# Optimization experiments

Hardware: AMD Instinct MI355X
Metric: run time of the kernel (lower is better)

## Reference

```python
import jax, jax.numpy as jnp
import numpy as np

LAMBDA_GEO = 0.5


def setup_inputs() -> dict:
    key = jax.random.key(0)
    embeddings = jax.random.normal(key, (4, 2048, 512), dtype=jnp.float32)
    return {"embeddings": embeddings}


def _geometric_loss(embeddings):
    b, s, d = embeddings.shape
    x = embeddings.reshape(b * s, d)  # [N, d]
    sq_norm = jnp.sum(x * x, axis=-1)  # [N]
    sq = sq_norm[:, None] + sq_norm[None, :] - 2.0 * (x @ x.T)  # [N, N]
    sq = jnp.maximum(sq, 0.0)
    dist = jnp.sqrt(sq)  # torch.cdist(p=2)
    return jnp.mean(jnp.exp(-dist * 0.1)) * 0.1


def reference(embeddings):
    geometric_loss = _geometric_loss(embeddings)
    total_geometric = LAMBDA_GEO * geometric_loss
    return geometric_loss, total_geometric
```

## Files before the change

kernel.cpp:

```cpp
#include <hip/hip_runtime.h>

#define NROWS 8192
#define DIM   512
#define NT    64
#define NTRI  (NT * (NT + 1) / 2)
#define NACC  64

using f32x4 = __attribute__((ext_vector_type(4))) float;

__device__ __forceinline__ unsigned char f2e4m3(float x) {
    unsigned ux = __float_as_uint(x);
    unsigned s  = (ux >> 24) & 0x80u;
    float a = __uint_as_float(ux & 0x7FFFFFFFu);
    a = fminf(a, 448.0f);
    unsigned ua = __float_as_uint(a);
    int eb = (int)(ua >> 23);
    if (eb < 121) eb = 121;
    float step  = __uint_as_float((unsigned)(eb - 3) << 23);
    float istep = __uint_as_float((unsigned)(257 - eb) << 23);
    float q = rintf(a * istep) * step;
    q = fminf(q, 448.0f);
    if (q < 0.001953125f)
        return (unsigned char)s;
    unsigned uq = __float_as_uint(q);
    int eq = (int)(uq >> 23) - 127;
    unsigned byte;
    if (eq < -6) byte = (unsigned)(q * 512.0f);
    else         byte = (unsigned)((eq + 7) << 3) | ((uq >> 20) & 7u);
    return (unsigned char)(s | byte);
}

__global__ __launch_bounds__(256) void norm_convert_kernel(
    const float* __restrict__ X, unsigned char* __restrict__ Xq,
    float* __restrict__ norms, float* __restrict__ acc)
{
    const int tid  = threadIdx.x;
    const int lane = tid & 63;
    const int w    = tid >> 6;
    const int row  = blockIdx.x * 4 + w;

    if (blockIdx.x == 0 && tid < NACC) acc[tid] = 0.0f;

    const float* xr = X + (size_t)row * DIM + lane * 8;
    float4 v0 = *(const float4*)xr;
    float4 v1 = *(const float4*)(xr + 4);

    float s = 0.0f;
    s = fmaf(v0.x, v0.x, s); s = fmaf(v0.y, v0.y, s);
    s = fmaf(v0.z, v0.z, s); s = fmaf(v0.w, v0.w, s);
    s = fmaf(v1.x, v1.x, s); s = fmaf(v1.y, v1.y, s);
    s = fmaf(v1.z, v1.z, s); s = fmaf(v1.w, v1.w, s);

    union { unsigned char b[8]; uint2 v; } pk;
    pk.b[0] = f2e4m3(v0.x); pk.b[1] = f2e4m3(v0.y);
    pk.b[2] = f2e4m3(v0.z); pk.b[3] = f2e4m3(v0.w);
    pk.b[4] = f2e4m3(v1.x); pk.b[5] = f2e4m3(v1.y);
    pk.b[6] = f2e4m3(v1.z); pk.b[7] = f2e4m3(v1.w);

    const int slab = lane >> 3;
    const int cpos = (lane & 7) ^ (row & 7);
    *(uint2*)(Xq + (size_t)row * DIM + slab * 64 + cpos * 8) = pk.v;

    #pragma unroll
    for (int off = 32; off > 0; off >>= 1) s += __shfl_down(s, off, 64);
    if (lane == 0) norms[row] = s;
}

__global__ __launch_bounds__(256, 4) void pair_loss_gemm_kernel(
    const unsigned char* __restrict__ Xq, const float* __restrict__ norms,
    float* __restrict__ acc)
{
    __shared__ __align__(16) char As0[8192];
    __shared__ __align__(16) char As1[8192];
    __shared__ __align__(16) char Bs0[8192];
    __shared__ __align__(16) char Bs1[8192];
    __shared__ float wsum[4];

    int t = blockIdx.x, bi = 0;
    while (t >= (NT - bi)) { t -= (NT - bi); bi++; }
    const int bj = bi + t;

    const int tid  = threadIdx.x;
    const int lane = tid & 63;
    const int w    = tid >> 6;

    const int rowA = bi * 128;
    const int rowB = bj * 128;

    f32x4 accv[4][4];
    const f32x4 zero = {0.0f, 0.0f, 0.0f, 0.0f};
    #pragma unroll
    for (int a = 0; a < 4; a++)
        #pragma unroll
        for (int b = 0; b < 4; b++) accv[a][b] = zero;

    const int r0 = tid >> 1;
    const int h0 = tid & 1;
    const int wb = r0 * 64 + h0 * 32;
    const unsigned char* gA = Xq + (size_t)(rowA + r0) * DIM + h0 * 32;
    const unsigned char* gB = Xq + (size_t)(rowB + r0) * DIM + h0 * 32;

    const int fr  = lane & 15;
    const int q   = lane >> 4;
    const int fo0 = fr * 64 + ((q ^ (fr & 7)) * 8);
    const int wr  = (w & 1) * 64;
    const int wc  = (w >> 1) * 64;

    {
        uint4 pa0 = *(const uint4*)gA;
        uint4 pa1 = *(const uint4*)(gA + 16);
        uint4 pb0 = *(const uint4*)gB;
        uint4 pb1 = *(const uint4*)(gB + 16);
        *(uint4*)(As0 + wb)      = pa0;
        *(uint4*)(As0 + wb + 16) = pa1;
        *(uint4*)(Bs0 + wb)      = pb0;
        *(uint4*)(Bs0 + wb + 16) = pb1;
    }
    __syncthreads();

    char* curA = As0; char* nxtA = As1;
    char* curB = Bs0; char* nxtB = Bs1;

    #pragma unroll 1
    for (int k = 0; k < 8; k++) {
        uint4 pa0, pa1, pb0, pb1;
        const bool more = (k < 7);
        if (more) {
            const int k0 = (k + 1) * 64;
            pa0 = *(const uint4*)(gA + k0);
            pa1 = *(const uint4*)(gA + k0 + 16);
            pb0 = *(const uint4*)(gB + k0);
            pb1 = *(const uint4*)(gB + k0 + 16);
        }

        #pragma unroll
        for (int s = 0; s < 2; s++) {
            const int fo = fo0 ^ (s << 5);
            long af[4], bf[4];
            #pragma unroll
            for (int a = 0; a < 4; a++)
                af[a] = *(const long*)(curA + (wr + a * 16) * 64 + fo);
            #pragma unroll
            for (int b = 0; b < 4; b++)
                bf[b] = *(const long*)(curB + (wc + b * 16) * 64 + fo);
            #pragma unroll
            for (int a = 0; a < 4; a++)
                #pragma unroll
                for (int b = 0; b < 4; b++)
                    accv[a][b] = __builtin_amdgcn_mfma_f32_16x16x32_fp8_fp8(
                        af[a], bf[b], accv[a][b], 0, 0, 0);
        }

        if (more) {
            *(uint4*)(nxtA + wb)      = pa0;
            *(uint4*)(nxtA + wb + 16) = pa1;
            *(uint4*)(nxtB + wb)      = pb0;
            *(uint4*)(nxtB + wb + 16) = pb1;
            __syncthreads();
            char* tA = curA; curA = nxtA; nxtA = tA;
            char* tB = curB; curB = nxtB; nxtB = tB;
        }
    }

    const float wgt = (bi == bj) ? 1.0f : 2.0f;
    float lsum = 0.0f;
    #pragma unroll
    for (int a = 0; a < 4; a++) {
        const int gi0 = rowA + wr + a * 16 + (lane >> 4) * 4;
        #pragma unroll
        for (int b = 0; b < 4; b++) {
            const int gj = rowB + wc + b * 16 + (lane & 15);
            const float nj = norms[gj];
            #pragma unroll
            for (int r = 0; r < 4; r++) {
                const int gi = gi0 + r;
                float sq = fmaf(-2.0f, accv[a][b][r], norms[gi] + nj);
                sq = fmaxf(sq, 0.0f);
                float term = __expf(-0.1f * sqrtf(sq));
                if (gi == gj) term = 1.0f;
                lsum += term;
            }
        }
    }
    lsum *= wgt;
    #pragma unroll
    for (int off = 32; off > 0; off >>= 1) lsum += __shfl_down(lsum, off, 64);
    if (lane == 0) wsum[w] = lsum;
    __syncthreads();
    if (tid == 0)
        atomicAdd(&acc[blockIdx.x & (NACC - 1)],
                  wsum[0] + wsum[1] + wsum[2] + wsum[3]);
}

__global__ void finalize_kernel(const float* __restrict__ acc,
                                float* __restrict__ out)
{
    const int lane = threadIdx.x;
    float s = (lane < NACC) ? acc[lane] : 0.0f;
    #pragma unroll
    for (int off = 32; off > 0; off >>= 1) s += __shfl_down(s, off, 64);
    if (lane == 0) {
        const float inv = 1.0f / ((float)NROWS * (float)NROWS);
        float loss = s * inv * 0.1f;
        out[0] = loss;
        out[1] = 0.5f * loss;
    }
}

extern "C" void kernel_launch(void* const* d_in, const int* in_sizes, int n_in,
                              void* d_out, int out_size, void* d_ws, size_t ws_size,
                              hipStream_t stream)
{
    const float* X = (const float*)d_in[0];
    float* out = (float*)d_out;

    char* ws = (char*)d_ws;
    float*         acc   = (float*)ws;
    float*         norms = (float*)(ws + 1024);
    unsigned char* Xq    = (unsigned char*)(ws + 1024 + 32768);

    norm_convert_kernel<<<NROWS / 4, 256, 0, stream>>>(X, Xq, norms, acc);
    pair_loss_gemm_kernel<<<NTRI, 256, 0, stream>>>(Xq, norms, acc);
    finalize_kernel<<<1, 64, 0, stream>>>(acc, out);
}
```

Baseline: 105.1 us.

## Stage FP8 tiles with direct global-to-LDS async loads and hoist fragment reads

Replaces the register-staged global loads and LDS stores in the pair GEMM with global_load_lds 16-byte async copies straight into the double-buffered shared tiles. The swizzle changes to key on row>>1 so the lane-linear async layout still avoids bank conflicts, and all LDS fragment reads for a K step are hoisted ahead of the MFMA loop. This removes VGPR staging and explicit ds_write instructions. It relies on the __syncthreads and waitcnt behaviour to make the async copies complete before use, and holding more fragment registers live may lower occupancy.

New measurement: 105.2 us. No clear change (+0.1%).

```diff
diff --git a/kernel.cpp b/kernel.cpp
--- a/kernel.cpp
+++ b/kernel.cpp
@@ -7,6 +7,13 @@
 #define NACC  64
 
 using f32x4 = __attribute__((ext_vector_type(4))) float;
+
+typedef __attribute__((address_space(1))) const void* as1_cvptr;
+typedef __attribute__((address_space(3))) void*       as3_vptr;
+
+__device__ __forceinline__ void async16(const void* g, void* l) {
+    __builtin_amdgcn_global_load_lds((as1_cvptr)g, (as3_vptr)l, 16, 0, 0);
+}
 
 __device__ __forceinline__ unsigned char f2e4m3(float x) {
     unsigned ux = __float_as_uint(x);
@@ -58,7 +65,7 @@
     pk.b[6] = f2e4m3(v1.z); pk.b[7] = f2e4m3(v1.w);
 
     const int slab = lane >> 3;
-    const int cpos = (lane & 7) ^ (row & 7);
+    const int cpos = (lane & 7) ^ ((row >> 1) & 7);
     *(uint2*)(Xq + (size_t)row * DIM + slab * 64 + cpos * 8) = pk.v;
 
     #pragma unroll
@@ -94,28 +101,23 @@
         #pragma unroll
         for (int b = 0; b < 4; b++) accv[a][b] = zero;
 
-    const int r0 = tid >> 1;
-    const int h0 = tid & 1;
-    const int wb = r0 * 64 + h0 * 32;
-    const unsigned char* gA = Xq + (size_t)(rowA + r0) * DIM + h0 * 32;
-    const unsigned char* gB = Xq + (size_t)(rowB + r0) * DIM + h0 * 32;
+    const int i0 = w * 128 + lane;
+    const int rr = i0 >> 2;
+    const int sl = i0 & 3;
+    const unsigned char* gAl = Xq + (size_t)(rowA + rr) * DIM + sl * 16;
+    const unsigned char* gBl = Xq + (size_t)(rowB + rr) * DIM + sl * 16;
+    const int ldw = w * 2048;
 
     const int fr  = lane & 15;
     const int q   = lane >> 4;
-    const int fo0 = fr * 64 + ((q ^ (fr & 7)) * 8);
+    const int fo0 = fr * 64 + ((q ^ ((fr >> 1) & 7)) * 8);
     const int wr  = (w & 1) * 64;
     const int wc  = (w >> 1) * 64;
 
-    {
-        uint4 pa0 = *(const uint4*)gA;
-        uint4 pa1 = *(const uint4*)(gA + 16);
-        uint4 pb0 = *(const uint4*)gB;
-        uint4 pb1 = *(const uint4*)(gB + 16);
-        *(uint4*)(As0 + wb)      = pa0;
-        *(uint4*)(As0 + wb + 16) = pa1;
-        *(uint4*)(Bs0 + wb)      = pb0;
-        *(uint4*)(Bs0 + wb + 16) = pb1;
-    }
+    async16(gAl,        As0 + ldw);
+    async16(gAl + 8192, As0 + ldw + 1024);
+    async16(gBl,        Bs0 + ldw);
+    async16(gBl + 8192, Bs0 + ldw + 1024);
     __syncthreads();
 
     char* curA = As0; char* nxtA = As1;
@@ -123,39 +125,37 @@
 
     #pragma unroll 1
     for (int k = 0; k < 8; k++) {
-        uint4 pa0, pa1, pb0, pb1;
+        long afr[2][4], bfr[2][4];
+        #pragma unroll
+        for (int s = 0; s < 2; s++) {
+            const int fo = fo0 ^ (s << 5);
+            #pragma unroll
+            for (int a = 0; a < 4; a++)
+                afr[s][a] = *(const long*)(curA + (wr + a * 16) * 64 + fo);
+            #pragma unroll
+            for (int b = 0; b < 4; b++)
+                bfr[s][b] = *(const long*)(curB + (wc + b * 16) * 64 + fo);
+        }
+
         const bool more = (k < 7);
         if (more) {
             const int k0 = (k + 1) * 64;
-            pa0 = *(const uint4*)(gA + k0);
-            pa1 = *(const uint4*)(gA + k0 + 16);
-            pb0 = *(const uint4*)(gB + k0);
-            pb1 = *(const uint4*)(gB + k0 + 16);
-        }
-
-        #pragma unroll
-        for (int s = 0; s < 2; s++) {
-            const int fo = fo0 ^ (s << 5);
-            long af[4], bf[4];
-            #pragma unroll
-            for (int a = 0; a < 4; a++)
-                af[a] = *(const long*)(curA + (wr + a * 16) * 64 + fo);
-            #pragma unroll
-            for (int b = 0; b < 4; b++)
-                bf[b] = *(const long*)(curB + (wc + b * 16) * 64 + fo);
+            async16(gAl + k0,        nxtA + ldw);
+            async16(gAl + k0 + 8192, nxtA + ldw + 1024);
+            async16(gBl + k0,        nxtB + ldw);
+            async16(gBl + k0 + 8192, nxtB + ldw + 1024);
+        }
+
+        #pragma unroll
+        for (int s = 0; s < 2; s++)
             #pragma unroll
             for (int a = 0; a < 4; a++)
                 #pragma unroll
                 for (int b = 0; b < 4; b++)
                     accv[a][b] = __builtin_amdgcn_mfma_f32_16x16x32_fp8_fp8(
-                        af[a], bf[b], accv[a][b], 0, 0, 0);
-        }
+                        afr[s][a], bfr[s][b], accv[a][b], 0, 0, 0);
 
         if (more) {
-            *(uint4*)(nxtA + wb)      = pa0;
-            *(uint4*)(nxtA + wb + 16) = pa1;
-            *(uint4*)(nxtB + wb)      = pb0;
-            *(uint4*)(nxtB + wb + 16) = pb1;
             __syncthreads();
             char* tA = curA; curA = nxtA; nxtA = tA;
             char* tB = curB; curB = nxtB; nxtB = tB;
```
